# Optimization experiments

Measured on AMD Instinct MI355X. Metric: run time of the kernel, lower is better.

## Reference

```python
import jax, jax.numpy as jnp
import numpy as np

B, S, D = 2, 2048, 1024
NH, NKV = 16, 4
HD = D // NH
KVD = NKV * HD
NE, MM = 8, 4
INTER = MM * D // NE  # 512
ROPE_BASE = 10000.0
ALPHA, BETA, GATE, DT = 0.95, 0.3, 0.1, 0.1
MU_MIN, MU_MAX, VMAX = 0.5, 1.5, 3.0


def rms_norm(x):
    # torch F.rms_norm with eps=None -> finfo(dtype).eps, no learned weight
    return x * jax.lax.rsqrt(jnp.mean(x * x, axis=-1, keepdims=True) + jnp.finfo(x.dtype).eps)


def rope_tables(seq_len, dtype):
    inv_freq = 1.0 / ROPE_BASE ** (jnp.arange(0, HD, 2, dtype=jnp.float32) / HD)
    t = jnp.arange(seq_len, dtype=jnp.float32)
    freqs = jnp.outer(t, inv_freq)  # [S, HD/2]
    return jnp.cos(freqs).astype(dtype)[None, None], jnp.sin(freqs).astype(dtype)[None, None]


def apply_rotary(x, cos, sin):
    half = x.shape[-1] // 2
    x1, x2 = x[..., :half], x[..., half:]
    return jnp.concatenate((x1 * cos + x2 * sin, -x1 * sin + x2 * cos), axis=-1)


def attention(n, cq_w, ck_w, cv_w, proj_w, q_gain):
    q = jnp.einsum('bsd,od->bso', n, cq_w).reshape(B, S, NH, HD).transpose(0, 2, 1, 3)
    k = jnp.einsum('bsd,od->bso', n, ck_w).reshape(B, S, NKV, HD).transpose(0, 2, 1, 3)
    v = jnp.einsum('bsd,od->bso', n, cv_w).reshape(B, S, NKV, HD).transpose(0, 2, 1, 3)
    q, k = rms_norm(q), rms_norm(k)
    cos, sin = rope_tables(S, q.dtype)
    q, k = apply_rotary(q, cos, sin), apply_rotary(k, cos, sin)
    q = q * q_gain[None, :, None, None]
    rep = NH // NKV  # GQA: repeat kv heads
    k = jnp.repeat(k, rep, axis=1)
    v = jnp.repeat(v, rep, axis=1)
    scale = 1.0 / np.sqrt(HD).astype(np.float32)
    scores = jnp.einsum('bhqd,bhkd->bhqk', q, k) * scale
    causal = jnp.tril(jnp.ones((S, S), bool))
    scores = jnp.where(causal[None, None], scores, jnp.finfo(scores.dtype).min)
    probs = jax.nn.softmax(scores, axis=-1)
    y = jnp.einsum('bhqk,bhkd->bhqd', probs, v)
    y = y.transpose(0, 2, 1, 3).reshape(B, S, D)
    return jnp.einsum('bsd,od->bso', y, proj_w)


def moe(m, gate_up, down, eids):
    # faithful to TokenRoutedMLP: dense per-expert GEMM, masked accumulate
    flat = m.reshape(-1, D)
    fids = eids.reshape(-1)
    out = jnp.zeros_like(flat)
    for e in range(NE):
        gu = flat @ gate_up[e]                       # [T, 2*INTER]
        g, u = gu[:, :INTER], gu[:, INTER:]
        h = (jax.nn.silu(g) * u) @ down[e]           # [T, D]
        out = out + h * (fids == e)[:, None].astype(flat.dtype)
    return out.reshape(B, S, D)


def setup_inputs():
    key = jax.random.key(0)
    ks = jax.random.split(key, 10)
    w = lambda k, shape: jax.random.normal(k, shape, jnp.float32) * 0.02
    return {
        'x': jax.random.normal(ks[0], (B, S, D), jnp.float32),
        'x0': jax.random.normal(ks[1], (B, S, D), jnp.float32),
        'vel': jnp.zeros((B, S, D), jnp.float32),
        'resid_mix': jnp.stack((jnp.ones(D, jnp.float32), jnp.zeros(D, jnp.float32))),
        'attn_scale': jnp.ones(D, jnp.float32),
        'mlp_scale': jnp.ones(D, jnp.float32),
        'cq_w': w(ks[2], (D, D)),
        'ck_w': w(ks[3], (KVD, D)),
        'cv_w': w(ks[4], (KVD, D)),
        'proj_w': w(ks[5], (D, D)),
        'q_gain': jnp.ones(NH, jnp.float32),
        'mu': jnp.full((D,), 1.0, jnp.float32),
        'gate_up': w(ks[6], (NE, D, 2 * INTER)),
        'down': w(ks[7], (NE, INTER, D)),
        'eids': jax.random.randint(ks[8], (B, S), 0, NE),
    }


def reference(x, x0, vel, resid_mix, attn_scale, mlp_scale, cq_w, ck_w, cv_w, proj_w, q_gain, mu, gate_up, down, eids):
    x = resid_mix[0][None, None, :] * x + resid_mix[1][None, None, :] * x0
    n = rms_norm(x)
    x = x + attn_scale[None, None, :] * attention(n, cq_w, ck_w, cv_w, proj_w, q_gain)
    # PID dynamics
    mu_c = jnp.clip(mu, MU_MIN, MU_MAX)
    v_next = jnp.clip(ALPHA * vel - BETA * (x - mu_c[None, None, :]), -VMAX, VMAX)
    x = x + DT * GATE * v_next
    x = x + mlp_scale[None, None, :] * moe(rms_norm(x), gate_up, down, eids)
    return x, v_next
```

## Files before the change

kernel.cpp:

```cpp
#include <hip/hip_runtime.h>
#include <hip/hip_bf16.h>
#include <math.h>

#define NBATCH 2
#define NSEQ   2048
#define NDIM   1024
#define NHEAD  16
#define NKVH   4
#define HDIM   64
#define KVD    256
#define NEXP   8
#define NINTER 512
#define NTOK   (NBATCH*NSEQ)
#define QKVN   1536
#define MAXTILE 40
#define RMS_EPS 1.1920929e-07f
#define LN_10000 9.210340371976184f
#define QSCALE (0.125f * 1.44269504088896f)
#define DEFER_THR 11.5f
#define LOG2E 1.44269504088896f

typedef __attribute__((ext_vector_type(8))) short bf16x8;
typedef __attribute__((ext_vector_type(4))) short short4v;
typedef __attribute__((ext_vector_type(4))) float f32x4;

__device__ __forceinline__ short f2b(float f) {
  return __builtin_bit_cast(short, (__bf16)f);
}
__device__ __forceinline__ float b2f(short s) {
  unsigned u = ((unsigned)(unsigned short)s) << 16;
  return __builtin_bit_cast(float, u);
}
__device__ __forceinline__ float ex2(float x) {
  float r; asm("v_exp_f32 %0, %1" : "=v"(r) : "v"(x)); return r;
}
__device__ __forceinline__ void load_lds16(const short* g, short* l) {
  __builtin_amdgcn_global_load_lds((const __attribute__((address_space(1))) void*)g,
                                   (__attribute__((address_space(3))) void*)l, 16, 0, 0);
}

__device__ __forceinline__ float wred64(float v) {
#pragma unroll
  for (int m = 32; m >= 1; m >>= 1) v += __shfl_xor(v, m);
  return v;
}

__global__ __launch_bounds__(256) void k_w_prep(
    const float* __restrict__ cq, const float* __restrict__ ck,
    const float* __restrict__ cv, const float* __restrict__ pw,
    const float* __restrict__ gate_up,
    short* __restrict__ wqkv, short* __restrict__ wproj, short* __restrict__ wgu_t) {
  __shared__ short T[64*66];
  const int bid = blockIdx.x;
  const int t = threadIdx.x;
  if (bid < 2560) {
    const int row = bid;
    const int c = t * 4;
    const float* src; short* dst;
    if (row < 1024)      { src = cq + (size_t)row*NDIM;        dst = wqkv + (size_t)row*NDIM; }
    else if (row < 1280) { src = ck + (size_t)(row-1024)*NDIM; dst = wqkv + (size_t)row*NDIM; }
    else if (row < 1536) { src = cv + (size_t)(row-1280)*NDIM; dst = wqkv + (size_t)row*NDIM; }
    else                 { src = pw + (size_t)(row-1536)*NDIM; dst = wproj + (size_t)(row-1536)*NDIM; }
    float4 v = *(const float4*)(src + c);
    short4v o = {f2b(v.x), f2b(v.y), f2b(v.z), f2b(v.w)};
    *(short4v*)(dst + c) = o;
  } else {
    const int b2 = bid - 2560;
    const int kt = b2 & 15, nt = (b2 >> 4) & 15, e = b2 >> 8;
    const float* ie = gate_up + (size_t)e*1024*1024 + (size_t)(kt*64)*1024 + nt*64;
    short* we = wgu_t + (size_t)e*1024*1024;
    const int r = t >> 4, c = (t & 15) * 4;
#pragma unroll
    for (int p = 0; p < 4; ++p) {
      float4 v = *(const float4*)(ie + (size_t)(p*16 + r)*1024 + c);
      T[(p*16 + r)*66 + c + 0] = f2b(v.x);
      T[(p*16 + r)*66 + c + 1] = f2b(v.y);
      T[(p*16 + r)*66 + c + 2] = f2b(v.z);
      T[(p*16 + r)*66 + c + 3] = f2b(v.w);
    }
    __syncthreads();
#pragma unroll
    for (int p = 0; p < 4; ++p) {
      int rr = p*16 + r;
      int R = nt*64 + rr;
      int Rn = (R < 512) ? ((R & ~15)*2 + (R & 15))
                         : (((R - 512) & ~15)*2 + 16 + (R & 15));
      short4v o = {T[(c+0)*66 + rr], T[(c+1)*66 + rr], T[(c+2)*66 + rr], T[(c+3)*66 + rr]};
      *(short4v*)(we + (size_t)Rn*1024 + kt*64 + c) = o;
    }
  }
}

__global__ __launch_bounds__(256) void k_w_transpose(
    const float* __restrict__ in, short* __restrict__ outp, int KIN, int NIN) {
  __shared__ short T[64*66];
  const int kt = blockIdx.x, nt = blockIdx.y, e = blockIdx.z;
  const float* ie = in + (size_t)e*KIN*NIN + (size_t)(kt*64)*NIN + nt*64;
  short* oe = outp + (size_t)e*NIN*KIN + (size_t)(nt*64)*KIN + kt*64;
  const int t = threadIdx.x;
  const int r = t >> 4, c = (t & 15) * 4;
#pragma unroll
  for (int p = 0; p < 4; ++p) {
    float4 v = *(const float4*)(ie + (size_t)(p*16 + r)*NIN + c);
    T[(p*16 + r)*66 + c + 0] = f2b(v.x);
    T[(p*16 + r)*66 + c + 1] = f2b(v.y);
    T[(p*16 + r)*66 + c + 2] = f2b(v.z);
    T[(p*16 + r)*66 + c + 3] = f2b(v.w);
  }
  __syncthreads();
#pragma unroll
  for (int p = 0; p < 4; ++p) {
    int rr = p*16 + r;
    short4v o = {T[(c+0)*66 + rr], T[(c+1)*66 + rr], T[(c+2)*66 + rr], T[(c+3)*66 + rr]};
    *(short4v*)(oe + (size_t)rr*KIN + c) = o;
  }
}

__global__ __launch_bounds__(256) void k_resid_rms(
    const float* __restrict__ x, const float* __restrict__ x0,
    const float* __restrict__ rmix, short* __restrict__ xr, short* __restrict__ nrm) {
  const int row = blockIdx.x;
  const int t = threadIdx.x;
  const int d = t * 4;
  const size_t base = (size_t)row * NDIM + d;
  float4 a  = *(const float4*)(x  + base);
  float4 b  = *(const float4*)(x0 + base);
  float4 m0 = *(const float4*)(rmix + d);
  float4 m1 = *(const float4*)(rmix + NDIM + d);
  float4 r;
  r.x = m0.x*a.x + m1.x*b.x;
  r.y = m0.y*a.y + m1.y*b.y;
  r.z = m0.z*a.z + m1.z*b.z;
  r.w = m0.w*a.w + m1.w*b.w;
  float ss = r.x*r.x + r.y*r.y + r.z*r.z + r.w*r.w;
  ss = wred64(ss);
  __shared__ float wsum[4];
  if ((t & 63) == 0) wsum[t >> 6] = ss;
  __syncthreads();
  float tot = wsum[0] + wsum[1] + wsum[2] + wsum[3];
  float rms = rsqrtf(tot * (1.0f/NDIM) + RMS_EPS);
  short4v xo = {f2b(r.x), f2b(r.y), f2b(r.z), f2b(r.w)};
  short4v no = {f2b(r.x*rms), f2b(r.y*rms), f2b(r.z*rms), f2b(r.w*rms)};
  *(short4v*)(xr + base) = xo;
  *(short4v*)(nrm + base) = no;
}

template <int MODE>
__global__ __launch_bounds__(256) void k_gemm_mfma(
    const short* __restrict__ A, int lda,
    const short* __restrict__ Bw, int K, int N,
    short* __restrict__ Cb, float* __restrict__ Cf, int ldc,
    const int* __restrict__ rowmap, const int* __restrict__ tiletab,
    const int* __restrict__ meta, const float* __restrict__ mscale) {
  __shared__ short sA[2][128*32];
  __shared__ short sB[2][128*32];
  int row0, end = 0x7fffffff, e = 0;
  if (MODE == 0) {
    row0 = blockIdx.y * 128;
  } else {
    e = tiletab[2*blockIdx.y];
    if (e < 0) return;
    row0 = tiletab[2*blockIdx.y + 1];
    end = meta[1 + e];
  }
  const int t = threadIdx.x;
  const int w = t >> 6, l = t & 63;
  const int wr = (w >> 1) * 64, wc = (w & 1) * 64;
  const int lrow = l & 15, lk8 = (l >> 4) * 8;
  const int srow0 = w*16 + (l >> 2);
  const int scol = (l & 3) * 8;
  const short* Bp = Bw + (size_t)e * N * K + (size_t)(blockIdx.x * 128) * K;
  const short* gA0;
  const short* gA1;
  if (MODE == 1 || MODE == 3) {
    int s0 = row0 + srow0;      if (s0 >= NTOK) s0 = NTOK - 1;
    int s1 = row0 + 64 + srow0; if (s1 >= NTOK) s1 = NTOK - 1;
    gA0 = A + (size_t)rowmap[s0] * lda + scol;
    gA1 = A + (size_t)rowmap[s1] * lda + scol;
  } else {
    gA0 = A + (size_t)(row0 + srow0) * lda + scol;
    gA1 = A + (size_t)(row0 + 64 + srow0) * lda + scol;
  }
  const short* gB0 = Bp + (size_t)srow0 * K + scol;
  const short* gB1 = Bp + (size_t)(64 + srow0) * K + scol;
  const int lo0 = (w*16)*32;
  const int lo1 = (64 + w*16)*32;
  f32x4 acc[4][4];
#pragma unroll
  for (int m = 0; m < 4; ++m)
#pragma unroll
    for (int n = 0; n < 4; ++n) acc[m][n] = 0.f;
  load_lds16(gA0, sA[0] + lo0);
  load_lds16(gA1, sA[0] + lo1);
  load_lds16(gB0, sB[0] + lo0);
  load_lds16(gB1, sB[0] + lo1);
  gA0 += 32; gA1 += 32; gB0 += 32; gB1 += 32;
  int cur = 0;
  for (int k0 = 0; k0 < K; k0 += 32) {
    __syncthreads();
    if (k0 + 32 < K) {
      load_lds16(gA0, sA[cur^1] + lo0);
      load_lds16(gA1, sA[cur^1] + lo1);
      load_lds16(gB0, sB[cur^1] + lo0);
      load_lds16(gB1, sB[cur^1] + lo1);
      gA0 += 32; gA1 += 32; gB0 += 32; gB1 += 32;
    }
    bf16x8 af[4], bfr[4];
#pragma unroll
    for (int m = 0; m < 4; ++m)
      af[m] = *(const bf16x8*)&sA[cur][(wr + m*16 + lrow)*32 + lk8];
#pragma unroll
    for (int n = 0; n < 4; ++n)
      bfr[n] = *(const bf16x8*)&sB[cur][(wc + n*16 + lrow)*32 + lk8];
    __builtin_amdgcn_s_setprio(1);
#pragma unroll
    for (int m = 0; m < 4; ++m)
#pragma unroll
      for (int n = 0; n < 4; ++n)
        acc[m][n] = __builtin_amdgcn_mfma_f32_16x16x32_bf16(af[m], bfr[n], acc[m][n], 0, 0, 0);
    __builtin_amdgcn_s_setprio(0);
    cur ^= 1;
  }
  const int col0 = blockIdx.x * 128;
  if (MODE <= 1) {
#pragma unroll
    for (int m = 0; m < 4; ++m) {
#pragma unroll
      for (int r = 0; r < 4; ++r) {
        int rr = row0 + wr + m*16 + (l >> 4)*4 + r;
        if (rr < end) {
#pragma unroll
          for (int n = 0; n < 4; ++n)
            Cb[(size_t)rr * ldc + col0 + wc + n*16 + lrow] = f2b(acc[m][n][r]);
        }
      }
    }
  } else if (MODE == 2) {
#pragma unroll
    for (int m = 0; m < 4; ++m) {
#pragma unroll
      for (int r = 0; r < 4; ++r) {
        int slot = row0 + wr + m*16 + (l >> 4)*4 + r;
        if (slot < end) {
          int tok = rowmap[slot];
#pragma unroll
          for (int n = 0; n < 4; ++n) {
            int cc = col0 + wc + n*16 + lrow;
            Cf[(size_t)tok * ldc + cc] += mscale[cc] * acc[m][n][r];
          }
        }
      }
    }
  } else {
    const int fbBase = (col0 + wc) >> 5;
#pragma unroll
    for (int m = 0; m < 4; ++m) {
#pragma unroll
      for (int r = 0; r < 4; ++r) {
        int slot = row0 + wr + m*16 + (l >> 4)*4 + r;
        if (slot < end) {
#pragma unroll
          for (int p = 0; p < 2; ++p) {
            float gg = acc[m][2*p][r], uu = acc[m][2*p+1][r];
            float sg = 1.0f / (1.0f + ex2(-LOG2E * gg));
            Cb[(size_t)slot * NINTER + (fbBase + p)*16 + lrow] = f2b(gg * sg * uu);
          }
        }
      }
    }
  }
}

__global__ __launch_bounds__(256) void k_qk_norm_rope(
    short* __restrict__ qkv, const float* __restrict__ q_gain, short* __restrict__ vbT) {
  __shared__ short T[64*72];
  const int row = blockIdx.x;
  const int t = threadIdx.x;
  const int w = t >> 6, lane = t & 63;
  const int s = row & (NSEQ - 1);
  const int fi = lane & 31;
  const float fr = (float)s * expf(-(float)fi * (LN_10000 / 32.0f));
  const float co = cosf(fr), si = sinf(fr);
#pragma unroll
  for (int h = w; h < NHEAD; h += 4) {
    short* p = qkv + (size_t)row*QKVN + h*HDIM + lane;
    float v = b2f(*p);
    float ssum = wred64(v*v);
    float rr = rsqrtf(ssum * (1.0f/HDIM) + RMS_EPS);
    float vn = v * rr;
    float partner = __shfl_xor(vn, 32);
    float o = (lane < 32) ? (vn*co + partner*si) : (vn*co - partner*si);
    *p = f2b(o * q_gain[h] * QSCALE);
  }
  if (w < NKVH) {
    short* p = qkv + (size_t)row*QKVN + 1024 + w*HDIM + lane;
    float v = b2f(*p);
    float ssum = wred64(v*v);
    float rr = rsqrtf(ssum * (1.0f/HDIM) + RMS_EPS);
    float vn = v * rr;
    float partner = __shfl_xor(vn, 32);
    float o = (lane < 32) ? (vn*co + partner*si) : (vn*co - partner*si);
    *p = f2b(o);
  }
  if (row < 256) {
    const int st = row & 31, kh = (row >> 5) & 3, b = row >> 7;
#pragma unroll
    for (int i = 0; i < 2; ++i) {
      int c = t + i*256;
      int sV = c >> 3, d0 = (c & 7) * 8;
      bf16x8 v = *(const bf16x8*)(qkv + (size_t)(b*NSEQ + st*64 + sV)*QKVN + 1280 + kh*HDIM + d0);
#pragma unroll
      for (int j = 0; j < 8; ++j) T[(d0 + j)*72 + sV] = v[j];
    }
    __syncthreads();
#pragma unroll
    for (int i = 0; i < 2; ++i) {
      int c = t + i*256;
      int d = c >> 3, s0 = (c & 7) * 8;
      *(bf16x8*)(vbT + (size_t)((b*NKVH + kh)*HDIM + d)*NSEQ + st*64 + s0) = *(bf16x8*)&T[d*72 + s0];
    }
  }
}

__global__ __launch_bounds__(256) void k_attn_mfma(
    const short* __restrict__ qkv, const short* __restrict__ vbT, short* __restrict__ y) {
  __shared__ short Ks[2][64*72];
  __shared__ short Vt[2][64*72];
  __shared__ short Ps[64*72];
  const int t = threadIdx.x;
  const int l = t & 63, w = t >> 6;
  const int lrow = l & 15, g = l >> 4, lk8 = g * 8;
  const int bid = blockIdx.x;
  int qt = bid & 15;
  const int h = (bid >> 4) & 15, b = bid >> 8;
  if (b & 1) qt = 15 - qt;
  const int kh = h >> 2;
  bf16x8 qf[2][2];
#pragma unroll
  for (int qra = 0; qra < 2; ++qra) {
    int qrow_g = b*NSEQ + qt*128 + qra*64 + w*16 + lrow;
#pragma unroll
    for (int hf = 0; hf < 2; ++hf)
      qf[qra][hf] = *(const bf16x8*)(qkv + (size_t)qrow_g*QKVN + h*HDIM + hf*32 + lk8);
  }
  const int r0a = t >> 3;
  const int d0a = (t & 7) * 8;
  const short* kgbase = qkv + 1024 + (size_t)kh*HDIM;
  const short* vgbase = vbT + (size_t)((b*NKVH + kh)*HDIM)*NSEQ;
  bf16x8 kr0, kr1, vr0, vr1;
#define LOADKV(KT) do { \
    kr0 = *(const bf16x8*)(kgbase + (size_t)(b*NSEQ + (KT)*64 + r0a)*QKVN + d0a); \
    kr1 = *(const bf16x8*)(kgbase + (size_t)(b*NSEQ + (KT)*64 + r0a + 32)*QKVN + d0a); \
    vr0 = *(const bf16x8*)(vgbase + (size_t)r0a*NSEQ + (KT)*64 + d0a); \
    vr1 = *(const bf16x8*)(vgbase + (size_t)(r0a + 32)*NSEQ + (KT)*64 + d0a); \
  } while (0)
  float m_i[2] = {-INFINITY, -INFINITY};
  float l_i[2] = {0.f, 0.f};
  f32x4 O[2][4];
#pragma unroll
  for (int qra = 0; qra < 2; ++qra)
#pragma unroll
    for (int db = 0; db < 4; ++db) O[qra][db] = 0.f;
  const int ktmax = 2*qt + 1;
  LOADKV(0);
  for (int kt = 0; kt <= ktmax; ++kt) {
    const int buf = kt & 1;
    *(bf16x8*)&Ks[buf][r0a*72 + d0a] = kr0;
    *(bf16x8*)&Ks[buf][(r0a + 32)*72 + d0a] = kr1;
    *(bf16x8*)&Vt[buf][r0a*72 + d0a] = vr0;
    *(bf16x8*)&Vt[buf][(r0a + 32)*72 + d0a] = vr1;
    __syncthreads();
    if (kt < ktmax) LOADKV(kt + 1);
    bf16x8 kf[4][2];
#pragma unroll
    for (int nb = 0; nb < 4; ++nb) {
      kf[nb][0] = *(const bf16x8*)&Ks[buf][(nb*16 + lrow)*72 + lk8];
      kf[nb][1] = *(const bf16x8*)&Ks[buf][(nb*16 + lrow)*72 + 32 + lk8];
    }
    const int qra0 = (kt == ktmax) ? 1 : 0;
    bf16x8 pf[2][2];
#pragma unroll
    for (int qra = 0; qra < 2; ++qra) {
      if (qra >= qra0) {
        f32x4 sc[4];
#pragma unroll
        for (int nb = 0; nb < 4; ++nb) sc[nb] = 0.f;
        __builtin_amdgcn_s_setprio(1);
#pragma unroll
        for (int nb = 0; nb < 4; ++nb) {
          sc[nb] = __builtin_amdgcn_mfma_f32_16x16x32_bf16(kf[nb][0], qf[qra][0], sc[nb], 0, 0, 0);
          sc[nb] = __builtin_amdgcn_mfma_f32_16x16x32_bf16(kf[nb][1], qf[qra][1], sc[nb], 0, 0, 0);
        }
        __builtin_amdgcn_s_setprio(0);
        if (kt >= 2*qt) {
          int qg = qt*128 + qra*64 + w*16 + lrow;
#pragma unroll
          for (int nb = 0; nb < 4; ++nb)
#pragma unroll
            for (int r = 0; r < 4; ++r)
              if (kt*64 + nb*16 + g*4 + r > qg) sc[nb][r] = -INFINITY;
        }
        float rm = sc[0][0];
#pragma unroll
        for (int nb = 0; nb < 4; ++nb)
#pragma unroll
          for (int r = 0; r < 4; ++r) rm = fmaxf(rm, sc[nb][r]);
        rm = fmaxf(rm, __shfl_xor(rm, 16));
        rm = fmaxf(rm, __shfl_xor(rm, 32));
        if (!__all(rm <= m_i[qra] + DEFER_THR)) {
          float mn = fmaxf(m_i[qra], rm);
          float fac = ex2(m_i[qra] - mn);
          l_i[qra] *= fac;
          m_i[qra] = mn;
#pragma unroll
          for (int r = 0; r < 4; ++r) {
            float ff = __shfl(fac, g*4 + r);
#pragma unroll
            for (int db = 0; db < 4; ++db) O[qra][db][r] *= ff;
          }
        }
        float rs = 0.f;
#pragma unroll
        for (int nb = 0; nb < 4; ++nb) {
#pragma unroll
          for (int r = 0; r < 4; ++r) {
            float p = ex2(sc[nb][r] - m_i[qra]);
            sc[nb][r] = p;
            rs += p;
          }
        }
        rs += __shfl_xor(rs, 16);
        rs += __shfl_xor(rs, 32);
        l_i[qra] += rs;
        short* prow = &Ps[(w*16 + lrow)*72];
#pragma unroll
        for (int nb = 0; nb < 4; ++nb) {
          short4v pk = {f2b(sc[nb][0]), f2b(sc[nb][1]), f2b(sc[nb][2]), f2b(sc[nb][3])};
          *(short4v*)(prow + nb*16 + g*4) = pk;
        }
        pf[qra][0] = *(const bf16x8*)&Ps[(w*16 + lrow)*72 + lk8];
        pf[qra][1] = *(const bf16x8*)&Ps[(w*16 + lrow)*72 + 32 + lk8];
      }
    }
    __builtin_amdgcn_s_setprio(1);
#pragma unroll
    for (int db = 0; db < 4; ++db) {
      bf16x8 vf0 = *(const bf16x8*)&Vt[buf][(db*16 + lrow)*72 + lk8];
      bf16x8 vf1 = *(const bf16x8*)&Vt[buf][(db*16 + lrow)*72 + 32 + lk8];
      if (qra0 == 0) {
        O[0][db] = __builtin_amdgcn_mfma_f32_16x16x32_bf16(pf[0][0], vf0, O[0][db], 0, 0, 0);
        O[0][db] = __builtin_amdgcn_mfma_f32_16x16x32_bf16(pf[0][1], vf1, O[0][db], 0, 0, 0);
      }
      O[1][db] = __builtin_amdgcn_mfma_f32_16x16x32_bf16(pf[1][0], vf0, O[1][db], 0, 0, 0);
      O[1][db] = __builtin_amdgcn_mfma_f32_16x16x32_bf16(pf[1][1], vf1, O[1][db], 0, 0, 0);
    }
    __builtin_amdgcn_s_setprio(0);
  }
#undef LOADKV
#pragma unroll
  for (int qra = 0; qra < 2; ++qra) {
    float linv = 1.0f / l_i[qra];
#pragma unroll
    for (int r = 0; r < 4; ++r) {
      float inv = __shfl(linv, g*4 + r);
      int rowo = b*NSEQ + qt*128 + qra*64 + w*16 + g*4 + r;
#pragma unroll
      for (int db = 0; db < 4; ++db)
        y[(size_t)rowo*NDIM + h*HDIM + db*16 + lrow] = f2b(O[qra][db][r] * inv);
    }
  }
}

__global__ __launch_bounds__(256) void k_fuse_vel(
    const short* __restrict__ xr, const short* __restrict__ aout,
    const float* __restrict__ vel, const float* __restrict__ ascale,
    const float* __restrict__ mu, float* __restrict__ out, short* __restrict__ mbuf) {
  const int row = blockIdx.x;
  const int t = threadIdx.x;
  const int d = t * 4;
  const size_t base = (size_t)row * NDIM + d;
  short4v a4 = *(const short4v*)(xr + base);
  short4v o4 = *(const short4v*)(aout + base);
  float4 vv = *(const float4*)(vel + base);
  float4 as = *(const float4*)(ascale + d);
  float4 mu4 = *(const float4*)(mu + d);
  float xs[4], vns[4];
  const float asl[4] = {as.x, as.y, as.z, as.w};
  const float mul[4] = {mu4.x, mu4.y, mu4.z, mu4.w};
  const float vvl[4] = {vv.x, vv.y, vv.z, vv.w};
#pragma unroll
  for (int i = 0; i < 4; ++i) {
    float x1 = b2f(a4[i]) + asl[i] * b2f(o4[i]);
    float muc = fminf(fmaxf(mul[i], 0.5f), 1.5f);
    float vn = fminf(fmaxf(0.95f*vvl[i] - 0.3f*(x1 - muc), -3.f), 3.f);
    xs[i] = x1 + 0.01f*vn;
    vns[i] = vn;
  }
  float4 x2 = {xs[0], xs[1], xs[2], xs[3]};
  float4 vnq = {vns[0], vns[1], vns[2], vns[3]};
  *(float4*)(out + base) = x2;
  *(float4*)(out + (size_t)NTOK*NDIM + base) = vnq;
  float ss = xs[0]*xs[0] + xs[1]*xs[1] + xs[2]*xs[2] + xs[3]*xs[3];
  ss = wred64(ss);
  __shared__ float wsum[4];
  if ((t & 63) == 0) wsum[t >> 6] = ss;
  __syncthreads();
  float tot = wsum[0] + wsum[1] + wsum[2] + wsum[3];
  float rms = rsqrtf(tot * (1.0f/NDIM) + RMS_EPS);
  short4v m4 = {f2b(xs[0]*rms), f2b(xs[1]*rms), f2b(xs[2]*rms), f2b(xs[3]*rms)};
  *(short4v*)(mbuf + base) = m4;
}

__global__ __launch_bounds__(256) void k_route(
    const int* __restrict__ eids, int* __restrict__ rowmap,
    int* __restrict__ tiletab, int* __restrict__ meta) {
  __shared__ int cnt[NEXP];
  __shared__ int ctr[NEXP];
  const int t = threadIdx.x;
  if (t < NEXP) cnt[t] = 0;
  __syncthreads();
  for (int i = t; i < NTOK; i += 256) atomicAdd(&cnt[eids[i]], 1);
  __syncthreads();
  if (t == 0) {
    int off = 0, tile = 0;
    for (int e = 0; e < NEXP; ++e) {
      ctr[e] = off;
      int nt_e = (cnt[e] + 127) >> 7;
      for (int j = 0; j < nt_e; ++j) { tiletab[2*tile] = e; tiletab[2*tile+1] = off + j*128; ++tile; }
      off += cnt[e];
      meta[1 + e] = off;
    }
    meta[0] = tile;
    for (int j = tile; j < MAXTILE; ++j) { tiletab[2*j] = -1; tiletab[2*j+1] = 0; }
  }
  __syncthreads();
  for (int i = t; i < NTOK; i += 256) {
    int e = eids[i];
    int slot = atomicAdd(&ctr[e], 1);
    rowmap[slot] = i;
  }
}

extern "C" void kernel_launch(void* const* d_in, const int* in_sizes, int n_in,
                              void* d_out, int out_size, void* d_ws, size_t ws_size,
                              hipStream_t stream) {
  const float* x      = (const float*)d_in[0];
  const float* x0     = (const float*)d_in[1];
  const float* vel    = (const float*)d_in[2];
  const float* rmix   = (const float*)d_in[3];
  const float* ascale = (const float*)d_in[4];
  const float* mscale = (const float*)d_in[5];
  const float* cq_w   = (const float*)d_in[6];
  const float* ck_w   = (const float*)d_in[7];
  const float* cv_w   = (const float*)d_in[8];
  const float* proj_w = (const float*)d_in[9];
  const float* q_gain = (const float*)d_in[10];
  const float* mu     = (const float*)d_in[11];
  const float* gate_up= (const float*)d_in[12];
  const float* down   = (const float*)d_in[13];
  const int*   eids   = (const int*)d_in[14];
  float* out = (float*)d_out;
  char* base = (char*)d_ws;

  const size_t MB = 1024*1024;
  short* wqkv  = (short*)base;
  short* wproj = (short*)(base + 3*MB);
  int*   rowmap  = (int*)(base + 5*MB);
  int*   tiletab = rowmap + NTOK;
  int*   meta    = tiletab + 2*MAXTILE;
  short* wgu_t = (short*)(base + 6*MB);
  short* xr    = (short*)(base + 22*MB);
  short* hbuf  = xr;
  short* nbuf  = (short*)(base + 30*MB);
  short* ybuf  = nbuf;
  short* mbuf  = nbuf;
  short* wdn_t = nbuf;
  short* qkv   = (short*)(base + 38*MB);
  short* aout  = qkv;
  short* vbT   = (short*)(base + 50*MB);

  k_w_prep<<<4608, 256, 0, stream>>>(cq_w, ck_w, cv_w, proj_w, gate_up, wqkv, wproj, wgu_t);
  k_resid_rms<<<NTOK, 256, 0, stream>>>(x, x0, rmix, xr, nbuf);
  k_gemm_mfma<0><<<dim3(QKVN/128, NTOK/128), 256, 0, stream>>>(
      nbuf, NDIM, wqkv, NDIM, QKVN, qkv, nullptr, QKVN, nullptr, nullptr, nullptr, nullptr);
  k_qk_norm_rope<<<NTOK, 256, 0, stream>>>(qkv, q_gain, vbT);
  k_attn_mfma<<<NBATCH*NHEAD*(NSEQ/128), 256, 0, stream>>>(qkv, vbT, ybuf);
  k_gemm_mfma<0><<<dim3(NDIM/128, NTOK/128), 256, 0, stream>>>(
      ybuf, NDIM, wproj, NDIM, NDIM, aout, nullptr, NDIM, nullptr, nullptr, nullptr, nullptr);
  k_fuse_vel<<<NTOK, 256, 0, stream>>>(xr, aout, vel, ascale, mu, out, mbuf);
  k_route<<<1, 256, 0, stream>>>(eids, rowmap, tiletab, meta);
  k_gemm_mfma<3><<<dim3(1024/128, MAXTILE), 256, 0, stream>>>(
      mbuf, NDIM, wgu_t, NDIM, 1024, hbuf, nullptr, NINTER, rowmap, tiletab, meta, nullptr);
  k_w_transpose<<<dim3(8, 16, 8), 256, 0, stream>>>(down, wdn_t, 512, 1024);
  k_gemm_mfma<2><<<dim3(NDIM/128, MAXTILE), 256, 0, stream>>>(
      hbuf, NINTER, wdn_t, NINTER, NDIM, nullptr, out, NDIM, rowmap, tiletab, meta, mscale);
}
```

Measured before the change: 221.7 us.

## Use direct global-to-LDS loads with XOR swizzle in attention; fold routing into fuse_vel

```diff
diff --git a/kernel.cpp b/kernel.cpp
--- a/kernel.cpp
+++ b/kernel.cpp
@@ -324,8 +324,8 @@
 
 __global__ __launch_bounds__(256) void k_attn_mfma(
     const short* __restrict__ qkv, const short* __restrict__ vbT, short* __restrict__ y) {
-  __shared__ short Ks[2][64*72];
-  __shared__ short Vt[2][64*72];
+  __shared__ short Ks[2][64*64];
+  __shared__ short Vt[2][64*64];
   __shared__ short Ps[64*72];
   const int t = threadIdx.x;
   const int l = t & 63, w = t >> 6;
@@ -343,16 +343,15 @@
     for (int hf = 0; hf < 2; ++hf)
       qf[qra][hf] = *(const bf16x8*)(qkv + (size_t)qrow_g*QKVN + h*HDIM + hf*32 + lk8);
   }
-  const int r0a = t >> 3;
-  const int d0a = (t & 7) * 8;
+  const int srow = w*8 + (l >> 3);
+  const int csw = ((l & 7) ^ (l >> 3)) * 8;
   const short* kgbase = qkv + 1024 + (size_t)kh*HDIM;
   const short* vgbase = vbT + (size_t)((b*NKVH + kh)*HDIM)*NSEQ;
-  bf16x8 kr0, kr1, vr0, vr1;
-#define LOADKV(KT) do { \
-    kr0 = *(const bf16x8*)(kgbase + (size_t)(b*NSEQ + (KT)*64 + r0a)*QKVN + d0a); \
-    kr1 = *(const bf16x8*)(kgbase + (size_t)(b*NSEQ + (KT)*64 + r0a + 32)*QKVN + d0a); \
-    vr0 = *(const bf16x8*)(vgbase + (size_t)r0a*NSEQ + (KT)*64 + d0a); \
-    vr1 = *(const bf16x8*)(vgbase + (size_t)(r0a + 32)*NSEQ + (KT)*64 + d0a); \
+#define GLOADKV(KT, BUF) do { \
+    load_lds16(kgbase + (size_t)(b*NSEQ + (KT)*64 + srow)*QKVN + csw,      &Ks[BUF][(w*8)*64]); \
+    load_lds16(kgbase + (size_t)(b*NSEQ + (KT)*64 + srow + 32)*QKVN + csw, &Ks[BUF][(w*8 + 32)*64]); \
+    load_lds16(vgbase + (size_t)srow*NSEQ + (KT)*64 + csw,                 &Vt[BUF][(w*8)*64]); \
+    load_lds16(vgbase + (size_t)(srow + 32)*NSEQ + (KT)*64 + csw,          &Vt[BUF][(w*8 + 32)*64]); \
   } while (0)
   float m_i[2] = {-INFINITY, -INFINITY};
   float l_i[2] = {0.f, 0.f};
@@ -362,20 +361,17 @@
 #pragma unroll
     for (int db = 0; db < 4; ++db) O[qra][db] = 0.f;
   const int ktmax = 2*qt + 1;
-  LOADKV(0);
+  GLOADKV(0, 0);
   for (int kt = 0; kt <= ktmax; ++kt) {
     const int buf = kt & 1;
-    *(bf16x8*)&Ks[buf][r0a*72 + d0a] = kr0;
-    *(bf16x8*)&Ks[buf][(r0a + 32)*72 + d0a] = kr1;
-    *(bf16x8*)&Vt[buf][r0a*72 + d0a] = vr0;
-    *(bf16x8*)&Vt[buf][(r0a + 32)*72 + d0a] = vr1;
-    __syncthreads();
-    if (kt < ktmax) LOADKV(kt + 1);
+    __syncthreads();
+    if (kt < ktmax) GLOADKV(kt + 1, buf ^ 1);
     bf16x8 kf[4][2];
 #pragma unroll
     for (int nb = 0; nb < 4; ++nb) {
-      kf[nb][0] = *(const bf16x8*)&Ks[buf][(nb*16 + lrow)*72 + lk8];
-      kf[nb][1] = *(const bf16x8*)&Ks[buf][(nb*16 + lrow)*72 + 32 + lk8];
+      int rsw = (lrow & 7);
+      kf[nb][0] = *(const bf16x8*)&Ks[buf][(nb*16 + lrow)*64 + ((g ^ rsw) * 8)];
+      kf[nb][1] = *(const bf16x8*)&Ks[buf][(nb*16 + lrow)*64 + (((4 + g) ^ rsw) * 8)];
     }
     const int qra0 = (kt == ktmax) ? 1 : 0;
     bf16x8 pf[2][2];
@@ -445,8 +441,9 @@
     __builtin_amdgcn_s_setprio(1);
 #pragma unroll
     for (int db = 0; db < 4; ++db) {
-      bf16x8 vf0 = *(const bf16x8*)&Vt[buf][(db*16 + lrow)*72 + lk8];
-      bf16x8 vf1 = *(const bf16x8*)&Vt[buf][(db*16 + lrow)*72 + 32 + lk8];
+      int rsw = (lrow & 7);
+      bf16x8 vf0 = *(const bf16x8*)&Vt[buf][(db*16 + lrow)*64 + ((g ^ rsw) * 8)];
+      bf16x8 vf1 = *(const bf16x8*)&Vt[buf][(db*16 + lrow)*64 + (((4 + g) ^ rsw) * 8)];
       if (qra0 == 0) {
         O[0][db] = __builtin_amdgcn_mfma_f32_16x16x32_bf16(pf[0][0], vf0, O[0][db], 0, 0, 0);
         O[0][db] = __builtin_amdgcn_mfma_f32_16x16x32_bf16(pf[0][1], vf1, O[0][db], 0, 0, 0);
@@ -456,7 +453,7 @@
     }
     __builtin_amdgcn_s_setprio(0);
   }
-#undef LOADKV
+#undef GLOADKV
 #pragma unroll
   for (int qra = 0; qra < 2; ++qra) {
     float linv = 1.0f / l_i[qra];
@@ -474,7 +471,9 @@
 __global__ __launch_bounds__(256) void k_fuse_vel(
     const short* __restrict__ xr, const short* __restrict__ aout,
     const float* __restrict__ vel, const float* __restrict__ ascale,
-    const float* __restrict__ mu, float* __restrict__ out, short* __restrict__ mbuf) {
+    const float* __restrict__ mu, float* __restrict__ out, short* __restrict__ mbuf,
+    const int* __restrict__ eids, int* __restrict__ rowmap,
+    int* __restrict__ tiletab, int* __restrict__ meta) {
   const int row = blockIdx.x;
   const int t = threadIdx.x;
   const int d = t * 4;
@@ -509,35 +508,31 @@
   float rms = rsqrtf(tot * (1.0f/NDIM) + RMS_EPS);
   short4v m4 = {f2b(xs[0]*rms), f2b(xs[1]*rms), f2b(xs[2]*rms), f2b(xs[3]*rms)};
   *(short4v*)(mbuf + base) = m4;
-}
-
-__global__ __launch_bounds__(256) void k_route(
-    const int* __restrict__ eids, int* __restrict__ rowmap,
-    int* __restrict__ tiletab, int* __restrict__ meta) {
-  __shared__ int cnt[NEXP];
-  __shared__ int ctr[NEXP];
-  const int t = threadIdx.x;
-  if (t < NEXP) cnt[t] = 0;
-  __syncthreads();
-  for (int i = t; i < NTOK; i += 256) atomicAdd(&cnt[eids[i]], 1);
-  __syncthreads();
-  if (t == 0) {
-    int off = 0, tile = 0;
-    for (int e = 0; e < NEXP; ++e) {
-      ctr[e] = off;
-      int nt_e = (cnt[e] + 127) >> 7;
-      for (int j = 0; j < nt_e; ++j) { tiletab[2*tile] = e; tiletab[2*tile+1] = off + j*128; ++tile; }
-      off += cnt[e];
-      meta[1 + e] = off;
-    }
-    meta[0] = tile;
-    for (int j = tile; j < MAXTILE; ++j) { tiletab[2*j] = -1; tiletab[2*j+1] = 0; }
-  }
-  __syncthreads();
-  for (int i = t; i < NTOK; i += 256) {
-    int e = eids[i];
-    int slot = atomicAdd(&ctr[e], 1);
-    rowmap[slot] = i;
+  if (blockIdx.x == 0) {
+    __shared__ int cnt[NEXP];
+    __shared__ int ctr[NEXP];
+    if (t < NEXP) cnt[t] = 0;
+    __syncthreads();
+    for (int i = t; i < NTOK; i += 256) atomicAdd(&cnt[eids[i]], 1);
+    __syncthreads();
+    if (t == 0) {
+      int off = 0, tile = 0;
+      for (int e = 0; e < NEXP; ++e) {
+        ctr[e] = off;
+        int nt_e = (cnt[e] + 127) >> 7;
+        for (int j = 0; j < nt_e; ++j) { tiletab[2*tile] = e; tiletab[2*tile+1] = off + j*128; ++tile; }
+        off += cnt[e];
+        meta[1 + e] = off;
+      }
+      meta[0] = tile;
+      for (int j = tile; j < MAXTILE; ++j) { tiletab[2*j] = -1; tiletab[2*j+1] = 0; }
+    }
+    __syncthreads();
+    for (int i = t; i < NTOK; i += 256) {
+      int e = eids[i];
+      int slot = atomicAdd(&ctr[e], 1);
+      rowmap[slot] = i;
+    }
   }
 }
 
@@ -587,8 +582,8 @@
   k_attn_mfma<<<NBATCH*NHEAD*(NSEQ/128), 256, 0, stream>>>(qkv, vbT, ybuf);
   k_gemm_mfma<0><<<dim3(NDIM/128, NTOK/128), 256, 0, stream>>>(
       ybuf, NDIM, wproj, NDIM, NDIM, aout, nullptr, NDIM, nullptr, nullptr, nullptr, nullptr);
-  k_fuse_vel<<<NTOK, 256, 0, stream>>>(xr, aout, vel, ascale, mu, out, mbuf);
-  k_route<<<1, 256, 0, stream>>>(eids, rowmap, tiletab, meta);
+  k_fuse_vel<<<NTOK, 256, 0, stream>>>(xr, aout, vel, ascale, mu, out, mbuf,
+                                       eids, rowmap, tiletab, meta);
   k_gemm_mfma<3><<<dim3(1024/128, MAXTILE), 256, 0, stream>>>(
       mbuf, NDIM, wgu_t, NDIM, 1024, hbuf, nullptr, NINTER, rowmap, tiletab, meta, nullptr);
   k_w_transpose<<<dim3(8, 16, 8), 256, 0, stream>>>(down, wdn_t, 512, 1024);
```

Result: no change. 224.0 us (+1.0%).
